# Kernel tuning notes

Measured on AMD Instinct MI355X. Metric: run time of the kernel, lower is better.

## Reference

```python
import jax, jax.numpy as jnp
import numpy as np

B, H, K, D = 4096, 512, 32, 20


def setup_inputs() -> dict:
    key = jax.random.key(0)
    k1, k2 = jax.random.split(key)
    hidden = jax.random.normal(k1, (B, H), dtype=jnp.float32)
    # cluster: soft assignment probabilities (rows sum to 1), like a softmax output
    c = jax.random.uniform(k2, (B, K), dtype=jnp.float32)
    cluster = c / jnp.sum(c, axis=-1, keepdims=True)
    return {"hidden": hidden, "cluster": cluster, "d": D}


def reference(hidden, cluster, d):
    # softHidden[b,h,k] = hidden[b,h] * cluster[b,k]
    soft_hidden = hidden[:, :, None] * cluster[:, None, :]          # [B,H,K]
    class_sums = jnp.sum(soft_hidden, axis=0)                        # [H,K] (code calls these "class_means" but they are sums)
    within = jnp.sum((soft_hidden - class_sums[None]) ** 2, axis=0)  # [H,K]
    # round() has zero gradient in torch; mirror that with stop_gradient
    counts = jax.lax.stop_gradient(jnp.round(jnp.sum(cluster, axis=0)))  # [K]

    m = class_sums.T   # [K,H]
    w = within.T       # [K,H]

    # all class pairs i<j (the nested Python loops, vectorized)
    i, j = jnp.triu_indices(K, k=1)   # each [P], P = K*(K-1)/2
    mi, mj = m[i], m[j]                               # [P,H]
    gm = (mi + mj) / 2.0
    between = (mi - gm) ** 2 * counts[i][:, None] + (mj - gm) ** 2 * counts[j][:, None]
    pair_within = w[i] + w[j]                         # [P,H]
    pair_count = counts[i] + counts[j]                # [P]

    d2 = pair_count - 2.0
    d2 = jnp.where(d2 == 0.0, d2 + 1e-5, d2)
    x = between / (between + pair_within)
    x = jnp.clip(x, 1e-37, 1.0 - 1e-5)
    # regularized incomplete beta I_x(d1/2, d2/2) with d1 = 1
    xbetainc = jax.scipy.special.betainc(0.5, (d2 / 2.0)[:, None], x)  # [P,H]

    top_k, _ = jax.lax.top_k(xbetainc, d)             # [P,d]
    per_pair = jnp.sum(jnp.log(top_k), axis=-1)       # [P]
    return -jnp.sum(per_pair)
```

## Files before the change

### kernel.cpp

```cpp
#include <hip/hip_runtime.h>
#include <math.h>

#define BB 4096
#define HH 512
#define KK 32
#define PAIRS ((KK * (KK - 1)) / 2)

constexpr int TH  = 16;
constexpr int NBB = 16;
constexpr int BC  = BB / NBB;
constexpr int SUB = 64;
constexpr int RP  = TH + 1;

struct TabE {
    float v[2048];
    constexpr TabE() : v{} {
        double c = 1.0; v[0] = 1.0f;
        for (int j = 1; j < 2048; ++j) { c *= (2.0*j - 1.0) / (2.0*j); v[j] = (float)c; }
    }
};
struct TabO {
    float v[2048];
    constexpr TabO() : v{} {
        double c = 1.0; v[0] = 1.0f;
        for (int j = 1; j < 2048; ++j) { c *= (2.0*j) / (2.0*j + 1.0); v[j] = (float)c; }
    }
};
__device__ constexpr TabE tab_e{};
__device__ constexpr TabO tab_o{};

__global__ __launch_bounds__(256) void stage1_kernel(
    const float* __restrict__ hidden, const float* __restrict__ cluster,
    float* __restrict__ part_m, float* __restrict__ part_s,
    float* __restrict__ pcol, float* __restrict__ ctl)
{
    __shared__ float hid_s [SUB * TH];
    __shared__ float hid2_s[SUB * TH];
    __shared__ float clu_s [SUB * KK];
    __shared__ float red   [8 * KK * RP];
    __shared__ float cred  [8 * KK];

    const int t  = threadIdx.x;
    const int ty = t >> 5;
    const int tx = t & 31;
    const int h0 = blockIdx.x * TH;
    const int c  = blockIdx.y;
    const int bchunk = c * BC;

    if (blockIdx.x == 0 && c == 0 && t == 0) {
        ctl[0] = 0.0f;
        ((unsigned*)ctl)[1] = 0u;
    }

    float acc_m[TH], acc_s[TH];
#pragma unroll
    for (int i = 0; i < TH; ++i) { acc_m[i] = 0.f; acc_s[i] = 0.f; }
    float csum = 0.f;

    const float4* hid4 = (const float4*)hidden;
    const float4* clu4 = (const float4*)cluster;

    for (int sub = 0; sub < BC; sub += SUB) {
        const int b0 = bchunk + sub;
        {
            int r = t >> 2, q = t & 3;
            float4 v = hid4[(size_t)(b0 + r) * (HH / 4) + (h0 >> 2) + q];
            ((float4*)hid_s)[t] = v;
            float4 v2; v2.x = v.x*v.x; v2.y = v.y*v.y; v2.z = v.z*v.z; v2.w = v.w*v.w;
            ((float4*)hid2_s)[t] = v2;
        }
#pragma unroll
        for (int e = 0; e < 2; ++e) {
            int u = t + e * 256;
            int r = u >> 3, q = u & 7;
            ((float4*)clu_s)[u] = clu4[(size_t)(b0 + r) * (KK / 4) + q];
        }
        __syncthreads();

        const float4* h4 = (const float4*)hid_s;
        const float4* g4 = (const float4*)hid2_s;
#pragma unroll
        for (int s = 0; s < SUB / 8; ++s) {
            int r = s * 8 + ty;
            float cc = clu_s[r * KK + tx];
            float c2 = cc * cc;
            csum += cc;
            float4 a0 = h4[r*4+0], a1 = h4[r*4+1], a2 = h4[r*4+2], a3 = h4[r*4+3];
            float4 b0 = g4[r*4+0], b1 = g4[r*4+1], b2 = g4[r*4+2], b3 = g4[r*4+3];
            acc_m[0]  = fmaf(a0.x, cc, acc_m[0]);  acc_m[1]  = fmaf(a0.y, cc, acc_m[1]);
            acc_m[2]  = fmaf(a0.z, cc, acc_m[2]);  acc_m[3]  = fmaf(a0.w, cc, acc_m[3]);
            acc_m[4]  = fmaf(a1.x, cc, acc_m[4]);  acc_m[5]  = fmaf(a1.y, cc, acc_m[5]);
            acc_m[6]  = fmaf(a1.z, cc, acc_m[6]);  acc_m[7]  = fmaf(a1.w, cc, acc_m[7]);
            acc_m[8]  = fmaf(a2.x, cc, acc_m[8]);  acc_m[9]  = fmaf(a2.y, cc, acc_m[9]);
            acc_m[10] = fmaf(a2.z, cc, acc_m[10]); acc_m[11] = fmaf(a2.w, cc, acc_m[11]);
            acc_m[12] = fmaf(a3.x, cc, acc_m[12]); acc_m[13] = fmaf(a3.y, cc, acc_m[13]);
            acc_m[14] = fmaf(a3.z, cc, acc_m[14]); acc_m[15] = fmaf(a3.w, cc, acc_m[15]);
            acc_s[0]  = fmaf(b0.x, c2, acc_s[0]);  acc_s[1]  = fmaf(b0.y, c2, acc_s[1]);
            acc_s[2]  = fmaf(b0.z, c2, acc_s[2]);  acc_s[3]  = fmaf(b0.w, c2, acc_s[3]);
            acc_s[4]  = fmaf(b1.x, c2, acc_s[4]);  acc_s[5]  = fmaf(b1.y, c2, acc_s[5]);
            acc_s[6]  = fmaf(b1.z, c2, acc_s[6]);  acc_s[7]  = fmaf(b1.w, c2, acc_s[7]);
            acc_s[8]  = fmaf(b2.x, c2, acc_s[8]);  acc_s[9]  = fmaf(b2.y, c2, acc_s[9]);
            acc_s[10] = fmaf(b2.z, c2, acc_s[10]); acc_s[11] = fmaf(b2.w, c2, acc_s[11]);
            acc_s[12] = fmaf(b3.x, c2, acc_s[12]); acc_s[13] = fmaf(b3.y, c2, acc_s[13]);
            acc_s[14] = fmaf(b3.z, c2, acc_s[14]); acc_s[15] = fmaf(b3.w, c2, acc_s[15]);
        }
        __syncthreads();
    }

    cred[ty * KK + tx] = csum;
    __syncthreads();
    if (blockIdx.x == 0 && t < KK) {
        float v = 0.f;
#pragma unroll
        for (int g = 0; g < 8; ++g) v += cred[g * KK + t];
        pcol[c * KK + t] = v;
    }

#pragma unroll
    for (int hh = 0; hh < TH; ++hh)
        red[ty * (KK * RP) + tx * RP + hh] = acc_m[hh];
    __syncthreads();
    for (int u = t; u < KK * TH; u += 256) {
        int k = u >> 4, hh = u & 15;
        float v = 0.f;
#pragma unroll
        for (int g = 0; g < 8; ++g) v += red[g * (KK * RP) + k * RP + hh];
        part_m[((size_t)c * KK + k) * HH + h0 + hh] = v;
    }
    __syncthreads();
#pragma unroll
    for (int hh = 0; hh < TH; ++hh)
        red[ty * (KK * RP) + tx * RP + hh] = acc_s[hh];
    __syncthreads();
    for (int u = t; u < KK * TH; u += 256) {
        int k = u >> 4, hh = u & 15;
        float v = 0.f;
#pragma unroll
        for (int g = 0; g < 8; ++g) v += red[g * (KK * RP) + k * RP + hh];
        part_s[((size_t)c * KK + k) * HH + h0 + hh] = v;
    }
}

__device__ __forceinline__ float frcp(float x) {
#if __has_builtin(__builtin_amdgcn_rcpf)
    return __builtin_amdgcn_rcpf(x);
#else
    return 1.0f / x;
#endif
}
__device__ __forceinline__ float guardf(float t) {
    return (fabsf(t) < 1e-30f) ? 1e-30f : t;
}

__device__ float betacf_fast(float a, float b, float x)
{
    const float EPS = 1e-5f;
    float qab = a + b, qap = a + 1.0f, qam = a - 1.0f;
    float c = 1.0f;
    float d = frcp(guardf(1.0f - qab * x * frcp(qap)));
    float h = d;
    for (int m = 1; m <= 100; ++m) {
        float fm = (float)m, m2 = 2.0f * fm;
        float aa = fm * (b - fm) * x * frcp((qam + m2) * (a + m2));
        d = frcp(guardf(fmaf(aa, d, 1.0f)));
        c = guardf(fmaf(aa, frcp(c), 1.0f));
        h *= d * c;
        float aa2 = -(a + fm) * (qab + fm) * x * frcp((a + m2) * (qap + m2));
        d = frcp(guardf(fmaf(aa2, d, 1.0f)));
        c = guardf(fmaf(aa2, frcp(c), 1.0f));
        float del = d * c;
        h *= del;
        if (__all(fabsf(del - 1.0f) < EPS)) break;
    }
    return h;
}

__global__ __launch_bounds__(256) void stage2_kernel(
    const float* __restrict__ part_m, const float* __restrict__ part_s,
    const float* __restrict__ pcol, float* __restrict__ ctl,
    const int* __restrict__ dptr, float* __restrict__ out)
{
    __shared__ float xs[HH];

    const int t = threadIdx.x;
    const int w = t >> 6, lane = t & 63;
    const int p = blockIdx.x;

    int i = 0, rem = p;
    while (true) { int row = KK - 1 - i; if (rem < row) break; rem -= row; ++i; }
    const int j = i + 1 + rem;

    float ci = 0.f, cj = 0.f;
#pragma unroll
    for (int cc = 0; cc < NBB; ++cc) {
        ci += pcol[cc * KK + i];
        cj += pcol[cc * KK + j];
    }
    ci = roundf(ci); cj = roundf(cj);
    const float pc = ci + cj;
    float d2 = pc - 2.0f;
    if (d2 == 0.0f) d2 = 1e-5f;
    const float b = 0.5f * d2;

#pragma unroll
    for (int q = 0; q < 2; ++q) {
        int h = w * 128 + q * 64 + lane;
        float mi = 0.f, mj = 0.f, si = 0.f, sj = 0.f;
#pragma unroll
        for (int cc = 0; cc < NBB; ++cc) {
            size_t base = (size_t)cc * KK * HH;
            mi += part_m[base + (size_t)i * HH + h];
            mj += part_m[base + (size_t)j * HH + h];
            si += part_s[base + (size_t)i * HH + h];
            sj += part_s[base + (size_t)j * HH + h];
        }
        float wi = fmaf((float)(BB - 2) * mi, mi, si);
        float wj = fmaf((float)(BB - 2) * mj, mj, sj);
        float dm = 0.5f * (mi - mj);
        float between = dm * dm * pc;
        float denom = between + wi + wj;
        float x = between / denom;
        if (!(x >= 1e-37f)) x = 1e-37f;
        x = fminf(x, 1.0f - 1e-5f);
        xs[h] = x;
    }
    __syncthreads();
    if (w != 0) return;

    float lv[8];
#pragma unroll
    for (int q = 0; q < 8; ++q) lv[q] = xs[q * 64 + lane];

    const int d = *dptr;
    float myx = 0.004f;
    float lm = lv[0];
#pragma unroll
    for (int q = 1; q < 8; ++q) lm = fmaxf(lm, lv[q]);

    for (int r = 0; r < d; ++r) {
        float gm = lm;
#pragma unroll
        for (int off = 1; off < 64; off <<= 1)
            gm = fmaxf(gm, __shfl_xor(gm, off));
        unsigned long long msk = __ballot(lm == gm);
        int winner = __ffsll((unsigned long long)msk) - 1;
        if (lane == r) myx = gm;
        if (lane == winner) {
            bool done = false;
#pragma unroll
            for (int q = 0; q < 8; ++q)
                if (!done && lv[q] == gm) { lv[q] = -1.0f; done = true; }
            lm = lv[0];
#pragma unroll
            for (int q = 1; q < 8; ++q) lm = fmaxf(lm, lv[q]);
        }
    }

    float x  = myx;
    float u  = 1.0f - x;
    float sx = sqrtf(x);
    int nu = (int)(d2 + 0.5f);
    float L;
    if (nu >= 1 && nu <= 4094 && fabsf(d2 - (float)nu) < 1e-3f) {
        float u2 = u * u;
        if (nu & 1) {
            int terms = (nu - 1) >> 1;
            float S = 0.f;
            if (terms > 0) {
                float S0 = 0.f, S1 = 0.f, p0 = 1.f, p1 = u;
                int jj = 0;
                for (; jj + 1 < terms; jj += 2) {
                    S0 = fmaf(tab_o.v[jj],     p0, S0);
                    S1 = fmaf(tab_o.v[jj + 1], p1, S1);
                    p0 *= u2; p1 *= u2;
                }
                if (jj < terms) S0 = fmaf(tab_o.v[jj], p0, S0);
                S = S0 + S1;
            }
            float theta = asinf(fminf(sx, 1.0f));
            float A = 0.636619772367581343f * (theta + sx * sqrtf(u) * S);
            L = logf(fminf(A, 1.0f));
        } else {
            int terms = nu >> 1;
            float S0 = 0.f, S1 = 0.f, p0 = 1.f, p1 = u;
            int jj = 0;
            for (; jj + 1 < terms; jj += 2) {
                S0 = fmaf(tab_e.v[jj],     p0, S0);
                S1 = fmaf(tab_e.v[jj + 1], p1, S1);
                p0 *= u2; p1 *= u2;
            }
            if (jj < terms) S0 = fmaf(tab_e.v[jj], p0, S0);
            float A = sx * (S0 + S1);
            L = logf(fminf(A, 1.0f));
        }
    } else {
        const float a = 0.5f;
        const float lg = lgammaf(a + b) - lgammaf(b) - 0.57236494f;
        const float xsplit = (a + 1.0f) / (a + b + 2.0f);
        bool  brA = x < xsplit;
        float al  = brA ? a : b;
        float be  = brA ? b : a;
        float xx  = brA ? x : u;
        float cf  = betacf_fast(al, be, xx);
        float lbt = lg + 0.5f * logf(x) + b * logf(u);
        if (brA) {
            L = lbt + logf(2.0f * fmaxf(cf, 1e-30f));
        } else {
            float tt = expf(lbt) * cf / b;
            tt = fminf(tt, 0.99999988f);
            L = log1pf(-tt);
        }
    }

    float val = (lane < d) ? L : 0.0f;
#pragma unroll
    for (int off = 1; off < 64; off <<= 1) val += __shfl_xor(val, off);

    if (lane == 0) {
        atomicAdd(&ctl[0], -val);
        __threadfence();
        unsigned old = atomicAdd((unsigned*)ctl + 1, 1u);
        if (old == PAIRS - 1) {
            out[0] = atomicAdd(&ctl[0], 0.0f);
        }
    }
}

extern "C" void kernel_launch(void* const* d_in, const int* in_sizes, int n_in,
                              void* d_out, int out_size, void* d_ws, size_t ws_size,
                              hipStream_t stream)
{
    const float* hidden  = (const float*)d_in[0];
    const float* cluster = (const float*)d_in[1];
    const int*   dptr    = (const int*)d_in[2];

    float* part_m = (float*)d_ws;
    float* part_s = part_m + (size_t)NBB * KK * HH;
    float* pcol   = part_s + (size_t)NBB * KK * HH;
    float* ctl    = pcol + NBB * KK;

    dim3 g1(HH / TH, NBB);
    stage1_kernel<<<g1, 256, 0, stream>>>(hidden, cluster,
                                          part_m, part_s, pcol, ctl);
    stage2_kernel<<<PAIRS, 256, 0, stream>>>(part_m, part_s, pcol, ctl,
                                             dptr, (float*)d_out);
}
```

Baseline: 96.30 us.

## Fuse reduction and beta-inc stages into one kernel with flag-based block sync

Merges the two kernels into a single launch of PAIRS blocks. The first 256 blocks do the stage-1 batch reduction, with the batch split halved to 8 chunks so it fits in 256 blocks. Each of those blocks publishes a release flag, and every block spins until all flags are set before running the pairwise incomplete-beta and top-k step. The float atomic accumulation is replaced by per-pair partial results that the last block sums, which removes a kernel boundary and launch gap. The flags are set to a fixed magic value and never reset, so on repeated calls later blocks can pass the wait before the current stage-1 data is written. The spin-wait also relies on all blocks being co-resident on the device.

After: 162.3 us. 1.69x slower.

```diff
diff --git a/kernel.cpp b/kernel.cpp
--- a/kernel.cpp
+++ b/kernel.cpp
@@ -7,10 +7,12 @@
 #define PAIRS ((KK * (KK - 1)) / 2)
 
 constexpr int TH  = 16;
-constexpr int NBB = 16;
+constexpr int NBB = 8;
 constexpr int BC  = BB / NBB;
 constexpr int SUB = 64;
 constexpr int RP  = TH + 1;
+constexpr int S1B = (HH / TH) * NBB;
+constexpr unsigned MAGIC = 0x5F17BEEFu;
 
 struct TabE {
     float v[2048];
@@ -28,118 +30,6 @@
 };
 __device__ constexpr TabE tab_e{};
 __device__ constexpr TabO tab_o{};
-
-__global__ __launch_bounds__(256) void stage1_kernel(
-    const float* __restrict__ hidden, const float* __restrict__ cluster,
-    float* __restrict__ part_m, float* __restrict__ part_s,
-    float* __restrict__ pcol, float* __restrict__ ctl)
-{
-    __shared__ float hid_s [SUB * TH];
-    __shared__ float hid2_s[SUB * TH];
-    __shared__ float clu_s [SUB * KK];
-    __shared__ float red   [8 * KK * RP];
-    __shared__ float cred  [8 * KK];
-
-    const int t  = threadIdx.x;
-    const int ty = t >> 5;
-    const int tx = t & 31;
-    const int h0 = blockIdx.x * TH;
-    const int c  = blockIdx.y;
-    const int bchunk = c * BC;
-
-    if (blockIdx.x == 0 && c == 0 && t == 0) {
-        ctl[0] = 0.0f;
-        ((unsigned*)ctl)[1] = 0u;
-    }
-
-    float acc_m[TH], acc_s[TH];
-#pragma unroll
-    for (int i = 0; i < TH; ++i) { acc_m[i] = 0.f; acc_s[i] = 0.f; }
-    float csum = 0.f;
-
-    const float4* hid4 = (const float4*)hidden;
-    const float4* clu4 = (const float4*)cluster;
-
-    for (int sub = 0; sub < BC; sub += SUB) {
-        const int b0 = bchunk + sub;
-        {
-            int r = t >> 2, q = t & 3;
-            float4 v = hid4[(size_t)(b0 + r) * (HH / 4) + (h0 >> 2) + q];
-            ((float4*)hid_s)[t] = v;
-            float4 v2; v2.x = v.x*v.x; v2.y = v.y*v.y; v2.z = v.z*v.z; v2.w = v.w*v.w;
-            ((float4*)hid2_s)[t] = v2;
-        }
-#pragma unroll
-        for (int e = 0; e < 2; ++e) {
-            int u = t + e * 256;
-            int r = u >> 3, q = u & 7;
-            ((float4*)clu_s)[u] = clu4[(size_t)(b0 + r) * (KK / 4) + q];
-        }
-        __syncthreads();
-
-        const float4* h4 = (const float4*)hid_s;
-        const float4* g4 = (const float4*)hid2_s;
-#pragma unroll
-        for (int s = 0; s < SUB / 8; ++s) {
-            int r = s * 8 + ty;
-            float cc = clu_s[r * KK + tx];
-            float c2 = cc * cc;
-            csum += cc;
-            float4 a0 = h4[r*4+0], a1 = h4[r*4+1], a2 = h4[r*4+2], a3 = h4[r*4+3];
-            float4 b0 = g4[r*4+0], b1 = g4[r*4+1], b2 = g4[r*4+2], b3 = g4[r*4+3];
-            acc_m[0]  = fmaf(a0.x, cc, acc_m[0]);  acc_m[1]  = fmaf(a0.y, cc, acc_m[1]);
-            acc_m[2]  = fmaf(a0.z, cc, acc_m[2]);  acc_m[3]  = fmaf(a0.w, cc, acc_m[3]);
-            acc_m[4]  = fmaf(a1.x, cc, acc_m[4]);  acc_m[5]  = fmaf(a1.y, cc, acc_m[5]);
-            acc_m[6]  = fmaf(a1.z, cc, acc_m[6]);  acc_m[7]  = fmaf(a1.w, cc, acc_m[7]);
-            acc_m[8]  = fmaf(a2.x, cc, acc_m[8]);  acc_m[9]  = fmaf(a2.y, cc, acc_m[9]);
-            acc_m[10] = fmaf(a2.z, cc, acc_m[10]); acc_m[11] = fmaf(a2.w, cc, acc_m[11]);
-            acc_m[12] = fmaf(a3.x, cc, acc_m[12]); acc_m[13] = fmaf(a3.y, cc, acc_m[13]);
-            acc_m[14] = fmaf(a3.z, cc, acc_m[14]); acc_m[15] = fmaf(a3.w, cc, acc_m[15]);
-            acc_s[0]  = fmaf(b0.x, c2, acc_s[0]);  acc_s[1]  = fmaf(b0.y, c2, acc_s[1]);
-            acc_s[2]  = fmaf(b0.z, c2, acc_s[2]);  acc_s[3]  = fmaf(b0.w, c2, acc_s[3]);
-            acc_s[4]  = fmaf(b1.x, c2, acc_s[4]);  acc_s[5]  = fmaf(b1.y, c2, acc_s[5]);
-            acc_s[6]  = fmaf(b1.z, c2, acc_s[6]);  acc_s[7]  = fmaf(b1.w, c2, acc_s[7]);
-            acc_s[8]  = fmaf(b2.x, c2, acc_s[8]);  acc_s[9]  = fmaf(b2.y, c2, acc_s[9]);
-            acc_s[10] = fmaf(b2.z, c2, acc_s[10]); acc_s[11] = fmaf(b2.w, c2, acc_s[11]);
-            acc_s[12] = fmaf(b3.x, c2, acc_s[12]); acc_s[13] = fmaf(b3.y, c2, acc_s[13]);
-            acc_s[14] = fmaf(b3.z, c2, acc_s[14]); acc_s[15] = fmaf(b3.w, c2, acc_s[15]);
-        }
-        __syncthreads();
-    }
-
-    cred[ty * KK + tx] = csum;
-    __syncthreads();
-    if (blockIdx.x == 0 && t < KK) {
-        float v = 0.f;
-#pragma unroll
-        for (int g = 0; g < 8; ++g) v += cred[g * KK + t];
-        pcol[c * KK + t] = v;
-    }
-
-#pragma unroll
-    for (int hh = 0; hh < TH; ++hh)
-        red[ty * (KK * RP) + tx * RP + hh] = acc_m[hh];
-    __syncthreads();
-    for (int u = t; u < KK * TH; u += 256) {
-        int k = u >> 4, hh = u & 15;
-        float v = 0.f;
-#pragma unroll
-        for (int g = 0; g < 8; ++g) v += red[g * (KK * RP) + k * RP + hh];
-        part_m[((size_t)c * KK + k) * HH + h0 + hh] = v;
-    }
-    __syncthreads();
-#pragma unroll
-    for (int hh = 0; hh < TH; ++hh)
-        red[ty * (KK * RP) + tx * RP + hh] = acc_s[hh];
-    __syncthreads();
-    for (int u = t; u < KK * TH; u += 256) {
-        int k = u >> 4, hh = u & 15;
-        float v = 0.f;
-#pragma unroll
-        for (int g = 0; g < 8; ++g) v += red[g * (KK * RP) + k * RP + hh];
-        part_s[((size_t)c * KK + k) * HH + h0 + hh] = v;
-    }
-}
 
 __device__ __forceinline__ float frcp(float x) {
 #if __has_builtin(__builtin_amdgcn_rcpf)
@@ -175,16 +65,136 @@
     return h;
 }
 
-__global__ __launch_bounds__(256) void stage2_kernel(
-    const float* __restrict__ part_m, const float* __restrict__ part_s,
-    const float* __restrict__ pcol, float* __restrict__ ctl,
+__global__ __launch_bounds__(256) void fused_kernel(
+    const float* __restrict__ hidden, const float* __restrict__ cluster,
+    float* __restrict__ part_m, float* __restrict__ part_s,
+    float* __restrict__ pcol, float* __restrict__ pres,
+    unsigned* __restrict__ pctr, unsigned* __restrict__ flags,
     const int* __restrict__ dptr, float* __restrict__ out)
 {
+    __shared__ float hid_s [SUB * TH];
+    __shared__ float hid2_s[SUB * TH];
+    __shared__ float clu_s [SUB * KK];
+    __shared__ float red   [8 * KK * RP];
+    __shared__ float cred  [8 * KK];
     __shared__ float xs[HH];
 
-    const int t = threadIdx.x;
+    const int t   = threadIdx.x;
+    const int bid = blockIdx.x;
+
+    if (bid < S1B) {
+        const int ty = t >> 5;
+        const int tx = t & 31;
+        const int hx = bid & 31;
+        const int c  = bid >> 5;
+        const int h0 = hx * TH;
+        const int bchunk = c * BC;
+
+        if (bid == 0 && t == 0) *pctr = 0u;
+
+        float acc_m[TH], acc_s[TH];
+#pragma unroll
+        for (int i = 0; i < TH; ++i) { acc_m[i] = 0.f; acc_s[i] = 0.f; }
+        float csum = 0.f;
+
+        const float4* hid4 = (const float4*)hidden;
+        const float4* clu4 = (const float4*)cluster;
+
+        for (int sub = 0; sub < BC; sub += SUB) {
+            const int b0 = bchunk + sub;
+            {
+                int r = t >> 2, q = t & 3;
+                float4 v = hid4[(size_t)(b0 + r) * (HH / 4) + (h0 >> 2) + q];
+                ((float4*)hid_s)[t] = v;
+                float4 v2; v2.x=v.x*v.x; v2.y=v.y*v.y; v2.z=v.z*v.z; v2.w=v.w*v.w;
+                ((float4*)hid2_s)[t] = v2;
+            }
+#pragma unroll
+            for (int e = 0; e < 2; ++e) {
+                int u = t + e * 256;
+                int r = u >> 3, q = u & 7;
+                ((float4*)clu_s)[u] = clu4[(size_t)(b0 + r) * (KK / 4) + q];
+            }
+            __syncthreads();
+
+            const float4* h4 = (const float4*)hid_s;
+            const float4* g4 = (const float4*)hid2_s;
+#pragma unroll
+            for (int s = 0; s < SUB / 8; ++s) {
+                int r = s * 8 + ty;
+                float cc = clu_s[r * KK + tx];
+                float c2 = cc * cc;
+                csum += cc;
+                float4 a0=h4[r*4+0], a1=h4[r*4+1], a2=h4[r*4+2], a3=h4[r*4+3];
+                float4 q0=g4[r*4+0], q1=g4[r*4+1], q2=g4[r*4+2], q3=g4[r*4+3];
+                acc_m[0] =fmaf(a0.x,cc,acc_m[0]);  acc_m[1] =fmaf(a0.y,cc,acc_m[1]);
+                acc_m[2] =fmaf(a0.z,cc,acc_m[2]);  acc_m[3] =fmaf(a0.w,cc,acc_m[3]);
+                acc_m[4] =fmaf(a1.x,cc,acc_m[4]);  acc_m[5] =fmaf(a1.y,cc,acc_m[5]);
+                acc_m[6] =fmaf(a1.z,cc,acc_m[6]);  acc_m[7] =fmaf(a1.w,cc,acc_m[7]);
+                acc_m[8] =fmaf(a2.x,cc,acc_m[8]);  acc_m[9] =fmaf(a2.y,cc,acc_m[9]);
+                acc_m[10]=fmaf(a2.z,cc,acc_m[10]); acc_m[11]=fmaf(a2.w,cc,acc_m[11]);
+                acc_m[12]=fmaf(a3.x,cc,acc_m[12]); acc_m[13]=fmaf(a3.y,cc,acc_m[13]);
+                acc_m[14]=fmaf(a3.z,cc,acc_m[14]); acc_m[15]=fmaf(a3.w,cc,acc_m[15]);
+                acc_s[0] =fmaf(q0.x,c2,acc_s[0]);  acc_s[1] =fmaf(q0.y,c2,acc_s[1]);
+                acc_s[2] =fmaf(q0.z,c2,acc_s[2]);  acc_s[3] =fmaf(q0.w,c2,acc_s[3]);
+                acc_s[4] =fmaf(q1.x,c2,acc_s[4]);  acc_s[5] =fmaf(q1.y,c2,acc_s[5]);
+                acc_s[6] =fmaf(q1.z,c2,acc_s[6]);  acc_s[7] =fmaf(q1.w,c2,acc_s[7]);
+                acc_s[8] =fmaf(q2.x,c2,acc_s[8]);  acc_s[9] =fmaf(q2.y,c2,acc_s[9]);
+                acc_s[10]=fmaf(q2.z,c2,acc_s[10]); acc_s[11]=fmaf(q2.w,c2,acc_s[11]);
+                acc_s[12]=fmaf(q3.x,c2,acc_s[12]); acc_s[13]=fmaf(q3.y,c2,acc_s[13]);
+                acc_s[14]=fmaf(q3.z,c2,acc_s[14]); acc_s[15]=fmaf(q3.w,c2,acc_s[15]);
+            }
+            __syncthreads();
+        }
+
+        cred[ty * KK + tx] = csum;
+        __syncthreads();
+        if (hx == 0 && t < KK) {
+            float v = 0.f;
+#pragma unroll
+            for (int g = 0; g < 8; ++g) v += cred[g * KK + t];
+            pcol[c * KK + t] = v;
+        }
+
+#pragma unroll
+        for (int hh = 0; hh < TH; ++hh)
+            red[ty * (KK * RP) + tx * RP + hh] = acc_m[hh];
+        __syncthreads();
+        for (int u = t; u < KK * TH; u += 256) {
+            int k = u >> 4, hh = u & 15;
+            float v = 0.f;
+#pragma unroll
+            for (int g = 0; g < 8; ++g) v += red[g * (KK * RP) + k * RP + hh];
+            part_m[((size_t)c * KK + k) * HH + h0 + hh] = v;
+        }
+        __syncthreads();
+#pragma unroll
+        for (int hh = 0; hh < TH; ++hh)
+            red[ty * (KK * RP) + tx * RP + hh] = acc_s[hh];
+        __syncthreads();
+        for (int u = t; u < KK * TH; u += 256) {
+            int k = u >> 4, hh = u & 15;
+            float v = 0.f;
+#pragma unroll
+            for (int g = 0; g < 8; ++g) v += red[g * (KK * RP) + k * RP + hh];
+            part_s[((size_t)c * KK + k) * HH + h0 + hh] = v;
+        }
+
+        __threadfence();
+        __syncthreads();
+        if (t == 0)
+            __hip_atomic_store(&flags[bid], MAGIC, __ATOMIC_RELEASE,
+                               __HIP_MEMORY_SCOPE_AGENT);
+    }
+
+    while (__hip_atomic_load(&flags[t], __ATOMIC_RELAXED,
+                             __HIP_MEMORY_SCOPE_AGENT) != MAGIC)
+        __builtin_amdgcn_s_sleep(2);
+    __threadfence();
+    __syncthreads();
+
     const int w = t >> 6, lane = t & 63;
-    const int p = blockIdx.x;
+    const int p = bid;
 
     int i = 0, rem = p;
     while (true) { int row = KK - 1 - i; if (rem < row) break; rem -= row; ++i; }
@@ -316,13 +326,27 @@
 #pragma unroll
     for (int off = 1; off < 64; off <<= 1) val += __shfl_xor(val, off);
 
+    unsigned old = 0u;
     if (lane == 0) {
-        atomicAdd(&ctl[0], -val);
+        pres[p] = val;
         __threadfence();
-        unsigned old = atomicAdd((unsigned*)ctl + 1, 1u);
-        if (old == PAIRS - 1) {
-            out[0] = atomicAdd(&ctl[0], 0.0f);
-        }
+        old = __hip_atomic_fetch_add(pctr, 1u, __ATOMIC_ACQ_REL,
+                                     __HIP_MEMORY_SCOPE_AGENT);
+    }
+    old = __shfl(old, 0);
+    if (old == PAIRS - 1) {
+        __threadfence();
+        float s = 0.f;
+#pragma unroll
+        for (int q = 0; q < 8; ++q) {
+            int idx = q * 64 + lane;
+            if (idx < PAIRS)
+                s += __hip_atomic_load(&pres[idx], __ATOMIC_ACQUIRE,
+                                       __HIP_MEMORY_SCOPE_AGENT);
+        }
+#pragma unroll
+        for (int off = 1; off < 64; off <<= 1) s += __shfl_xor(s, off);
+        if (lane == 0) out[0] = -s;
     }
 }
 
@@ -334,14 +358,14 @@
     const float* cluster = (const float*)d_in[1];
     const int*   dptr    = (const int*)d_in[2];
 
-    float* part_m = (float*)d_ws;
-    float* part_s = part_m + (size_t)NBB * KK * HH;
-    float* pcol   = part_s + (size_t)NBB * KK * HH;
-    float* ctl    = pcol + NBB * KK;
-
-    dim3 g1(HH / TH, NBB);
-    stage1_kernel<<<g1, 256, 0, stream>>>(hidden, cluster,
-                                          part_m, part_s, pcol, ctl);
-    stage2_kernel<<<PAIRS, 256, 0, stream>>>(part_m, part_s, pcol, ctl,
-                                             dptr, (float*)d_out);
-}
+    float*    part_m = (float*)d_ws;
+    float*    part_s = part_m + (size_t)NBB * KK * HH;
+    float*    pcol   = part_s + (size_t)NBB * KK * HH;
+    float*    pres   = pcol + NBB * KK;
+    unsigned* pctr   = (unsigned*)(pres + PAIRS);
+    unsigned* flags  = pctr + 1;
+
+    fused_kernel<<<PAIRS, 256, 0, stream>>>(hidden, cluster,
+                                            part_m, part_s, pcol, pres,
+                                            pctr, flags, dptr, (float*)d_out);
+}
```
